# Performance work log

Measured on AMD Instinct MI355X. Metric: run time of the kernel, lower is better.

## Reference

```python
import jax, jax.numpy as jnp
import numpy as np

N = 100000
E = 1600000
G = 512  # number of graphs for pooling


def gcn_conv(x, W, b, src, dst, n):
    # PyG GCNConv: h = x @ W; symmetric deg^{-1/2} norm; scatter-add to dst; + bias
    h = x @ W                                            # [N, out]
    deg = jax.ops.segment_sum(jnp.ones(dst.shape, h.dtype), dst, num_segments=n)
    dinv = jnp.where(deg > 0, jax.lax.rsqrt(deg), 0.0)   # [N]
    norm = dinv[src] * dinv[dst]                         # [E']
    msg = norm[:, None] * h[src]                         # gather + scale, [E', out]
    out = jax.ops.segment_sum(msg, dst, num_segments=n)  # scatter-add
    return out + b


def setup_inputs() -> dict:
    key = jax.random.key(0)
    ks = jax.random.split(key, 8)
    x = jax.random.normal(ks[0], (N, 128), dtype=jnp.float32)
    edge_index = jax.random.randint(ks[1], (2, E), 0, N, dtype=jnp.int32)
    batch_index = jnp.sort(jax.random.randint(ks[2], (N,), 0, G, dtype=jnp.int32))
    W1 = jax.random.normal(ks[3], (128, 64), dtype=jnp.float32) * 0.1
    b1 = jax.random.normal(ks[4], (64,), dtype=jnp.float32) * 0.1
    W2 = jax.random.normal(ks[5], (64, 16), dtype=jnp.float32) * 0.1
    b2 = jax.random.normal(ks[6], (16,), dtype=jnp.float32) * 0.1
    return {"x": x, "edge_index": edge_index, "batch_index": batch_index,
            "W1": W1, "b1": b1, "W2": W2, "b2": b2}


def reference(x, edge_index, batch_index, W1, b1, W2, b2):
    n = x.shape[0]
    # add self-loops (PyG GCNConv default)
    loops = jnp.arange(n, dtype=edge_index.dtype)
    src = jnp.concatenate([edge_index[0], loops])
    dst = jnp.concatenate([edge_index[1], loops])

    h = jnp.tanh(gcn_conv(x, W1, b1, src, dst, n))
    h = jnp.tanh(gcn_conv(h, W2, b2, src, dst, n))

    # global_mean_pool over batch_index
    sums = jax.ops.segment_sum(h, batch_index, num_segments=G)            # [G, C]
    cnt = jax.ops.segment_sum(jnp.ones((n,), h.dtype), batch_index, num_segments=G)
    pooled = sums / jnp.maximum(cnt, 1.0)[:, None]
    return jax.nn.sigmoid(pooled)
```

## Files before the change

### kernel.cpp

```cpp
#include <hip/hip_runtime.h>
#include <hip/hip_bf16.h>

typedef float f4 __attribute__((ext_vector_type(4)));
typedef unsigned short us;
typedef unsigned int uint32;
typedef _Float16 h16;
typedef _Float16 h16x2 __attribute__((ext_vector_type(2)));

union h2u { uint32 u; h16 h[2]; h16x2 v; };
__device__ inline uint32 pack2h(float a, float b) { h2u x; x.h[0] = (h16)a; x.h[1] = (h16)b; return x.u; }

#define BSH 8
#define CHUNK 4096
#define CAP 6144

__global__ __launch_bounds__(256) void bscat_k(const int* __restrict__ src, const int* __restrict__ dst,
                                               int* __restrict__ bcur, unsigned int* __restrict__ bedge,
                                               const int* __restrict__ batch, int* __restrict__ gstart,
                                               int E, int B, int N, int G, int nchunk) {
    int tid = threadIdx.x;
    if (blockIdx.x >= nchunk) {
        int i = (blockIdx.x - nchunk) * 256 + tid;
        if (i >= N) return;
        int b = batch[i];
        int prev = (i == 0) ? -1 : batch[i - 1];
        for (int g = prev + 1; g <= b; ++g) gstart[g] = i;
        if (i == N - 1) {
            for (int g = b + 1; g <= G; ++g) gstart[g] = N;
        }
        return;
    }
    __shared__ int hist[512], lbase[512], cur2[512], gb[512];
    __shared__ int sa[512], sb[512];
    __shared__ unsigned int sedge[CHUNK];
    __shared__ unsigned short posb[CHUNK];
    int base = blockIdx.x * CHUNK;
    int n = min(CHUNK, E - base);
    for (int i = tid; i < 512; i += 256) hist[i] = 0;
    __syncthreads();
    for (int i = tid; i < n; i += 256) atomicAdd(&hist[dst[base + i] >> BSH], 1);
    __syncthreads();
    #pragma unroll
    for (int k = 0; k < 2; ++k) { int i = tid + k * 256; sa[i] = hist[i]; }
    __syncthreads();
    int* c = sa; int* nx = sb;
    for (int off = 1; off < 512; off <<= 1) {
        #pragma unroll
        for (int k = 0; k < 2; ++k) { int i = tid + k * 256; nx[i] = c[i] + (i >= off ? c[i - off] : 0); }
        __syncthreads();
        int* t = c; c = nx; nx = t;
    }
    #pragma unroll
    for (int k = 0; k < 2; ++k) {
        int i = tid + k * 256;
        int ex = c[i] - hist[i];
        lbase[i] = ex; cur2[i] = ex;
        if (i < B) gb[i] = hist[i] ? (i * CAP + atomicAdd(&bcur[i], hist[i])) : 0;
    }
    for (int t = tid; t < B; t += 256) {
        int e0 = lbase[t], e1 = e0 + hist[t];
        for (int j = e0; j < e1; ++j) posb[j] = (unsigned short)t;
    }
    __syncthreads();
    for (int i = tid; i < n; i += 256) {
        int d = dst[base + i];
        int s = src[base + i];
        int b = d >> BSH;
        int p = atomicAdd(&cur2[b], 1);
        sedge[p] = ((unsigned int)s << BSH) | (unsigned int)(d & ((1 << BSH) - 1));
    }
    __syncthreads();
    for (int i = tid; i < n; i += 256) {
        int b = posb[i];
        bedge[gb[b] + (i - lbase[b])] = sedge[i];
    }
}

__global__ __launch_bounds__(256) void bcsr_k(const unsigned int* __restrict__ bedge,
                                              const int* __restrict__ bcur,
                                              int* __restrict__ row_ptr, int* __restrict__ cnt,
                                              float* __restrict__ dinv, int* __restrict__ col,
                                              int N, int B) {
    __shared__ int hist[256], lofs[256], cur2[256];
    __shared__ int sa[256], sb[256];
    __shared__ int cols[CAP];
    int b = blockIdx.x, tid = threadIdx.x;
    int node0 = b << BSH;
    int g0 = b * CAP;
    int n = min(bcur[b], CAP);
    hist[tid] = 0;
    __syncthreads();
    for (int i = tid; i < n; i += 256) atomicAdd(&hist[bedge[g0 + i] & 255], 1);
    __syncthreads();
    sa[tid] = hist[tid];
    __syncthreads();
    int* c = sa; int* nx = sb;
    for (int off = 1; off < 256; off <<= 1) {
        nx[tid] = c[tid] + (tid >= off ? c[tid - off] : 0);
        __syncthreads();
        int* t = c; c = nx; nx = t;
    }
    int ex = c[tid] - hist[tid];
    lofs[tid] = ex; cur2[tid] = ex;
    int node = node0 + tid;
    if (node < N) {
        int deg = hist[tid];
        cnt[node] = deg;
        row_ptr[node] = g0 + ex;
        dinv[node] = rsqrtf((float)(deg + 1));
    }
    __syncthreads();
    for (int i = tid; i < n; i += 256) {
        unsigned int e = bedge[g0 + i];
        int p = atomicAdd(&cur2[e & 255], 1);
        if (p < CAP) cols[p] = (int)(e >> BSH);
    }
    __syncthreads();
    for (int i = tid; i < n; i += 256) col[g0 + i] = (i < CAP) ? cols[i] : 0;
}

__global__ __launch_bounds__(256) void gemm1_k(const float* __restrict__ x, const float* __restrict__ W1,
                                               const float* __restrict__ dinv, h16* __restrict__ hsh, int N) {
    __shared__ float xT[128][64];
    __shared__ float wS[128][64];
    const int tid = threadIdx.x;
    const int row0 = blockIdx.x * 64;

    {
        const f4* wsrc = (const f4*)W1;
        f4* wdst = (f4*)&wS[0][0];
        #pragma unroll
        for (int i = 0; i < 8; ++i) wdst[tid + i * 256] = wsrc[tid + i * 256];
    }
    {
        #pragma unroll
        for (int it = 0; it < 8; ++it) {
            int i = tid + it * 256;
            int r = i & 63;
            int k4 = (i >> 6) * 4;
            int row = row0 + r;
            f4 v = (f4)(0.0f);
            if (row < N) v = *(const f4*)(x + (size_t)row * 128 + k4);
            xT[k4 + 0][r] = v.x; xT[k4 + 1][r] = v.y;
            xT[k4 + 2][r] = v.z; xT[k4 + 3][r] = v.w;
        }
    }
    __syncthreads();

    const int rl = (tid & 15) * 4;
    const int c0 = (tid >> 4) * 4;
    f4 acc0 = (f4)(0.0f), acc1 = (f4)(0.0f), acc2 = (f4)(0.0f), acc3 = (f4)(0.0f);
    #pragma unroll 8
    for (int k = 0; k < 128; ++k) {
        f4 xa = *(const f4*)&xT[k][rl];
        f4 wb = *(const f4*)&wS[k][c0];
        acc0 += xa.x * wb;
        acc1 += xa.y * wb;
        acc2 += xa.z * wb;
        acc3 += xa.w * wb;
    }
    #pragma unroll
    for (int i = 0; i < 4; ++i) {
        int row = row0 + rl + i;
        if (row < N) {
            float di = dinv[row];
            f4 a = (i == 0) ? acc0 : (i == 1) ? acc1 : (i == 2) ? acc2 : acc3;
            a *= di;
            uint2 p;
            p.x = pack2h(a.x, a.y);
            p.y = pack2h(a.z, a.w);
            *(uint2*)(hsh + (size_t)row * 64 + c0) = p;
        }
    }
}

__global__ __launch_bounds__(256) void agg1_k(const h16* __restrict__ hsh, const int* __restrict__ row_ptr,
                                              const int* __restrict__ cnt, const int* __restrict__ col,
                                              const float* __restrict__ dinv, const float* __restrict__ b1,
                                              const float* __restrict__ W2, h16* __restrict__ h2sh, int N) {
    int wid = blockIdx.x * 4 + (threadIdx.x >> 6);
    int lane = threadIdx.x & 63;
    if (wid >= N) return;
    const int c16 = lane & 15;
    const int hh  = lane >> 4;
    float wreg[16];
    #pragma unroll
    for (int k = 0; k < 16; ++k) wreg[k] = W2[(hh * 16 + k) * 16 + c16];
    float bias = b1[lane];

    const int c2 = lane & 31;
    const int h  = lane >> 5;
    const uint32* rowbase = (const uint32*)hsh + c2;

    int beg = row_ptr[wid];
    int num = cnt[wid];
    float accx = 0.0f, accy = 0.0f;
    for (int e0 = 0; e0 < num; e0 += 64) {
        int rem = num - e0;
        int el = 0;
        if (lane < rem) el = col[beg + e0 + lane];
        int m = rem < 64 ? rem : 64;
        int e = 0;
        for (; e + 16 <= m; e += 16) {
            int s0 = __shfl(el, e + h);
            int s1 = __shfl(el, e + 2 + h);
            int s2 = __shfl(el, e + 4 + h);
            int s3 = __shfl(el, e + 6 + h);
            int s4 = __shfl(el, e + 8 + h);
            int s5 = __shfl(el, e + 10 + h);
            int s6 = __shfl(el, e + 12 + h);
            int s7 = __shfl(el, e + 14 + h);
            h2u u0, u1, u2, u3, u4, u5, u6, u7;
            u0.u = rowbase[(size_t)s0 * 32];
            u1.u = rowbase[(size_t)s1 * 32];
            u2.u = rowbase[(size_t)s2 * 32];
            u3.u = rowbase[(size_t)s3 * 32];
            u4.u = rowbase[(size_t)s4 * 32];
            u5.u = rowbase[(size_t)s5 * 32];
            u6.u = rowbase[(size_t)s6 * 32];
            u7.u = rowbase[(size_t)s7 * 32];
            h16x2 t01 = u0.v + u1.v;
            h16x2 t23 = u2.v + u3.v;
            h16x2 t45 = u4.v + u5.v;
            h16x2 t67 = u6.v + u7.v;
            h16x2 t03 = t01 + t23;
            h16x2 t47 = t45 + t67;
            h16x2 tt  = t03 + t47;
            accx += (float)tt[0];
            accy += (float)tt[1];
        }
        for (; e + 8 <= m; e += 8) {
            int s0 = __shfl(el, e + h);
            int s1 = __shfl(el, e + 2 + h);
            int s2 = __shfl(el, e + 4 + h);
            int s3 = __shfl(el, e + 6 + h);
            h2u u0, u1, u2, u3;
            u0.u = rowbase[(size_t)s0 * 32];
            u1.u = rowbase[(size_t)s1 * 32];
            u2.u = rowbase[(size_t)s2 * 32];
            u3.u = rowbase[(size_t)s3 * 32];
            accx += ((float)u0.h[0] + (float)u1.h[0]) + ((float)u2.h[0] + (float)u3.h[0]);
            accy += ((float)u0.h[1] + (float)u1.h[1]) + ((float)u2.h[1] + (float)u3.h[1]);
        }
        for (; e + 4 <= m; e += 4) {
            int s0 = __shfl(el, e + h);
            int s1 = __shfl(el, e + 2 + h);
            h2u u0, u1;
            u0.u = rowbase[(size_t)s0 * 32];
            u1.u = rowbase[(size_t)s1 * 32];
            accx += (float)u0.h[0] + (float)u1.h[0];
            accy += (float)u0.h[1] + (float)u1.h[1];
        }
        for (; e + 2 <= m; e += 2) {
            int s = __shfl(el, e + h);
            h2u u; u.u = rowbase[(size_t)s * 32];
            accx += (float)u.h[0];
            accy += (float)u.h[1];
        }
        if (e < m) {
            int s = __shfl(el, e);
            if (h == 0) {
                h2u u; u.u = rowbase[(size_t)s * 32];
                accx += (float)u.h[0];
                accy += (float)u.h[1];
            }
        }
    }
    accx += __shfl_xor(accx, 32);
    accy += __shfl_xor(accy, 32);
    float ra = __shfl(accx, lane >> 1);
    float rb = __shfl(accy, lane >> 1);
    float acc = (lane & 1) ? rb : ra;

    float di = dinv[wid];
    float self = (float)hsh[(size_t)wid * 64 + lane];
    float h1v = tanhf(di * (acc + self) + bias);

    float p = 0.0f;
    #pragma unroll
    for (int k = 0; k < 16; ++k) {
        float hv = __shfl(h1v, hh * 16 + k);
        p += hv * wreg[k];
    }
    p += __shfl_xor(p, 16);
    p += __shfl_xor(p, 32);
    if (lane < 16) h2sh[(size_t)wid * 16 + lane] = (h16)(di * p);
}

__global__ __launch_bounds__(256) void agg2_k(const h16* __restrict__ h2sh, const int* __restrict__ row_ptr,
                                              const int* __restrict__ cnt, const int* __restrict__ col,
                                              const float* __restrict__ dinv, const float* __restrict__ b2,
                                              h16* __restrict__ h2h, int N) {
    int t = blockIdx.x * 256 + threadIdx.x;
    int node = t >> 4;
    int c = t & 15;
    int sub = (threadIdx.x >> 4) & 3;
    if (node >= N) return;
    int beg = row_ptr[node];
    int num = cnt[node];
    float acc = 0.0f;
    for (int e0 = 0; e0 < num; e0 += 16) {
        int rem = num - e0;
        int el = 0;
        if (c < rem) el = col[beg + e0 + c];
        int m = rem < 16 ? rem : 16;
        int e = 0;
        for (; e + 4 <= m; e += 4) {
            int s0 = __shfl(el, (sub << 4) + e + 0);
            int s1 = __shfl(el, (sub << 4) + e + 1);
            int s2 = __shfl(el, (sub << 4) + e + 2);
            int s3 = __shfl(el, (sub << 4) + e + 3);
            float v0 = (float)h2sh[(size_t)s0 * 16 + c];
            float v1 = (float)h2sh[(size_t)s1 * 16 + c];
            float v2 = (float)h2sh[(size_t)s2 * 16 + c];
            float v3 = (float)h2sh[(size_t)s3 * 16 + c];
            acc += (v0 + v1) + (v2 + v3);
        }
        for (; e < m; ++e) {
            int s = __shfl(el, (sub << 4) + e);
            acc += (float)h2sh[(size_t)s * 16 + c];
        }
    }
    float di = dinv[node];
    float self = (float)h2sh[(size_t)node * 16 + c];
    h2h[(size_t)node * 16 + c] = (h16)tanhf(di * (acc + self) + b2[c]);
}

__global__ __launch_bounds__(256) void pool_seg_k(const h16* __restrict__ h2h, const int* __restrict__ gstart,
                                                  float* __restrict__ out) {
    __shared__ float sd[16][16];
    int g = blockIdx.x;
    int beg = gstart[g], end = gstart[g + 1];
    int tid = threadIdx.x;
    int c = tid & 15, r = tid >> 4;
    float acc = 0.0f;
    for (int i = beg + r; i < end; i += 16)
        acc += (float)h2h[(size_t)i * 16 + c];
    sd[r][c] = acc;
    __syncthreads();
    if (r < 8) sd[r][c] += sd[r + 8][c];
    __syncthreads();
    if (r < 4) sd[r][c] += sd[r + 4][c];
    __syncthreads();
    if (r < 2) sd[r][c] += sd[r + 2][c];
    __syncthreads();
    if (r == 0) {
        float m = (sd[0][c] + sd[1][c]) / fmaxf((float)(end - beg), 1.0f);
        out[g * 16 + c] = 1.0f / (1.0f + expf(-m));
    }
}

extern "C" void kernel_launch(void* const* d_in, const int* in_sizes, int n_in,
                              void* d_out, int out_size, void* d_ws, size_t ws_size,
                              hipStream_t stream) {
    const float* x     = (const float*)d_in[0];
    const int*   ei    = (const int*)d_in[1];
    const int*   batch = (const int*)d_in[2];
    const float* W1    = (const float*)d_in[3];
    const float* b1    = (const float*)d_in[4];
    const float* W2    = (const float*)d_in[5];
    const float* b2    = (const float*)d_in[6];
    float* out = (float*)d_out;

    const int N = in_sizes[2];
    const int E = in_sizes[1] / 2;
    const int G = out_size / 16;
    const int* src = ei;
    const int* dst = ei + E;

    const int B = (N + 255) >> 8;
    const int nchunk = (E + CHUNK - 1) / CHUNK;
    const int nbound = (N + 255) / 256;

    char* w = (char*)d_ws;
    int*   bcur     = (int*)w;    w += 512 * 4;
    int*   row_ptr  = (int*)w;    w += (size_t)N * 4;
    int*   cnt      = (int*)w;    w += (size_t)N * 4;
    float* dinv     = (float*)w;  w += (size_t)N * 4;
    int*   gstart   = (int*)w;    w += 528 * 4;
    int*   col      = (int*)w;    w += (size_t)B * CAP * 4;
    h16*   hsh      = (h16*)w;    w += (size_t)N * 64 * 2;
    h16*   h2sh     = (h16*)w;    w += (size_t)N * 16 * 2;
    h16*   h2h      = (h16*)w;    w += (size_t)N * 16 * 2;
    unsigned int* bedge = (unsigned int*)w;  w += (size_t)B * CAP * 4;

    hipMemsetAsync(bcur, 0, 512 * 4, stream);

    bscat_k <<<nchunk + nbound, 256, 0, stream>>>(src, dst, bcur, bedge, batch, gstart, E, B, N, G, nchunk);
    bcsr_k  <<<B, 256, 0, stream>>>(bedge, bcur, row_ptr, cnt, dinv, col, N, B);

    gemm1_k <<<(N + 63) / 64, 256, 0, stream>>>(x, W1, dinv, hsh, N);
    agg1_k  <<<(N + 3) / 4, 256, 0, stream>>>(hsh, row_ptr, cnt, col, dinv, b1, W2, h2sh, N);
    agg2_k  <<<((size_t)N * 16 + 255) / 256, 256, 0, stream>>>(h2sh, row_ptr, cnt, col, dinv, b2, h2h, N);
    pool_seg_k<<<G, 256, 0, stream>>>(h2h, gstart, out);
}
```

Baseline: 160.0 us.

## Use fp16 MFMA instructions for first-layer GEMM instead of FP32 FMA loop

Rewrites the x@W1 kernel to convert x and W1 to fp16 in shared memory with a padded or interleaved layout, then compute each 16x64 wave tile with mfma_f32_16x16x32_f16. This replaces the scalar fp32 outer-product loop and halves the shared memory footprint. In exchange, the inputs are rounded to fp16 before multiplication, and the output is written as scalar 2-byte stores rather than packed vector stores.

```diff
diff --git a/kernel.cpp b/kernel.cpp
--- a/kernel.cpp
+++ b/kernel.cpp
@@ -6,9 +6,10 @@
 typedef unsigned int uint32;
 typedef _Float16 h16;
 typedef _Float16 h16x2 __attribute__((ext_vector_type(2)));
+typedef _Float16 f16x8 __attribute__((ext_vector_type(8)));
+typedef float f32x4v __attribute__((ext_vector_type(4)));
 
 union h2u { uint32 u; h16 h[2]; h16x2 v; };
-__device__ inline uint32 pack2h(float a, float b) { h2u x; x.h[0] = (h16)a; x.h[1] = (h16)b; return x.u; }
 
 #define BSH 8
 #define CHUNK 4096
@@ -121,55 +122,58 @@
 
 __global__ __launch_bounds__(256) void gemm1_k(const float* __restrict__ x, const float* __restrict__ W1,
                                                const float* __restrict__ dinv, h16* __restrict__ hsh, int N) {
-    __shared__ float xT[128][64];
-    __shared__ float wS[128][64];
+    __shared__ h16 xS[64][136];
+    __shared__ h16 wS[8192];
     const int tid = threadIdx.x;
     const int row0 = blockIdx.x * 64;
 
-    {
-        const f4* wsrc = (const f4*)W1;
-        f4* wdst = (f4*)&wS[0][0];
-        #pragma unroll
-        for (int i = 0; i < 8; ++i) wdst[tid + i * 256] = wsrc[tid + i * 256];
-    }
-    {
-        #pragma unroll
-        for (int it = 0; it < 8; ++it) {
-            int i = tid + it * 256;
-            int r = i & 63;
-            int k4 = (i >> 6) * 4;
-            int row = row0 + r;
-            f4 v = (f4)(0.0f);
-            if (row < N) v = *(const f4*)(x + (size_t)row * 128 + k4);
-            xT[k4 + 0][r] = v.x; xT[k4 + 1][r] = v.y;
-            xT[k4 + 2][r] = v.z; xT[k4 + 3][r] = v.w;
-        }
-    }
-    __syncthreads();
-
-    const int rl = (tid & 15) * 4;
-    const int c0 = (tid >> 4) * 4;
-    f4 acc0 = (f4)(0.0f), acc1 = (f4)(0.0f), acc2 = (f4)(0.0f), acc3 = (f4)(0.0f);
-    #pragma unroll 8
-    for (int k = 0; k < 128; ++k) {
-        f4 xa = *(const f4*)&xT[k][rl];
-        f4 wb = *(const f4*)&wS[k][c0];
-        acc0 += xa.x * wb;
-        acc1 += xa.y * wb;
-        acc2 += xa.z * wb;
-        acc3 += xa.w * wb;
-    }
-    #pragma unroll
-    for (int i = 0; i < 4; ++i) {
-        int row = row0 + rl + i;
+    #pragma unroll
+    for (int i = 0; i < 32; ++i) {
+        int idx = tid + i * 256;
+        int k = idx >> 6, cc = idx & 63;
+        wS[(((k >> 3) * 64) + cc) * 8 + (k & 7)] = (h16)W1[idx];
+    }
+    #pragma unroll
+    for (int it = 0; it < 8; ++it) {
+        int i = tid + it * 256;
+        int r = i >> 5;
+        int k4 = (i & 31) * 4;
+        int row = row0 + r;
+        f4 v = (f4)(0.0f);
+        if (row < N) v = *(const f4*)(x + (size_t)row * 128 + k4);
+        xS[r][k4 + 0] = (h16)v.x; xS[r][k4 + 1] = (h16)v.y;
+        xS[r][k4 + 2] = (h16)v.z; xS[r][k4 + 3] = (h16)v.w;
+    }
+    __syncthreads();
+
+    const int wv = tid >> 6;
+    const int lane = tid & 63;
+    const int q = lane >> 4;
+    const int c = lane & 15;
+    f32x4v acc0 = {0.f, 0.f, 0.f, 0.f}, acc1 = acc0, acc2 = acc0, acc3 = acc0;
+    #pragma unroll
+    for (int kb = 0; kb < 4; ++kb) {
+        f16x8 a = *(const f16x8*)&xS[wv * 16 + c][kb * 32 + q * 8];
+        const h16* wb = &wS[(size_t)((kb * 4 + q) * 64) * 8];
+        f16x8 b0 = *(const f16x8*)&wb[(0 * 16 + c) * 8];
+        f16x8 b1 = *(const f16x8*)&wb[(1 * 16 + c) * 8];
+        f16x8 b2 = *(const f16x8*)&wb[(2 * 16 + c) * 8];
+        f16x8 b3 = *(const f16x8*)&wb[(3 * 16 + c) * 8];
+        acc0 = __builtin_amdgcn_mfma_f32_16x16x32_f16(a, b0, acc0, 0, 0, 0);
+        acc1 = __builtin_amdgcn_mfma_f32_16x16x32_f16(a, b1, acc1, 0, 0, 0);
+        acc2 = __builtin_amdgcn_mfma_f32_16x16x32_f16(a, b2, acc2, 0, 0, 0);
+        acc3 = __builtin_amdgcn_mfma_f32_16x16x32_f16(a, b3, acc3, 0, 0, 0);
+    }
+    #pragma unroll
+    for (int j = 0; j < 4; ++j) {
+        int row = row0 + wv * 16 + q * 4 + j;
         if (row < N) {
             float di = dinv[row];
-            f4 a = (i == 0) ? acc0 : (i == 1) ? acc1 : (i == 2) ? acc2 : acc3;
-            a *= di;
-            uint2 p;
-            p.x = pack2h(a.x, a.y);
-            p.y = pack2h(a.z, a.w);
-            *(uint2*)(hsh + (size_t)row * 64 + c0) = p;
+            size_t base = (size_t)row * 64;
+            hsh[base +  0 + c] = (h16)(acc0[j] * di);
+            hsh[base + 16 + c] = (h16)(acc1[j] * di);
+            hsh[base + 32 + c] = (h16)(acc2[j] * di);
+            hsh[base + 48 + c] = (h16)(acc3[j] * di);
         }
     }
 }
```

New measurement: 139.8 us. 12.6% less time.
